# Kernel tuning notes

Measured on AMD Instinct MI355X. Metric: run time of the kernel, lower is better.

Reference implementation:

```python
import jax, jax.numpy as jnp
import numpy as np

BLOCK_SIZE = 8
SELECT_TOPK = 32
HIDDEN = 512
CHANNELS = 384
NUM_HEADS = 8
B, H, W = 8, 64, 64


def setup_inputs() -> dict:
    key = jax.random.key(0)
    ks = jax.random.split(key, 8)
    num_block_tot = (H // BLOCK_SIZE) * (W // BLOCK_SIZE)
    bs2 = BLOCK_SIZE * BLOCK_SIZE
    x = jax.random.normal(ks[0], (B, H, W, CHANNELS), dtype=jnp.float32)
    aw = jax.random.normal(ks[1], (NUM_HEADS, B, num_block_tot, bs2, bs2 + SELECT_TOPK), dtype=jnp.float32)
    attn_weights = jax.nn.softmax(aw, axis=-1)  # module expects sum(-1)==1
    weights = jax.random.uniform(ks[2], (B, num_block_tot, SELECT_TOPK), dtype=jnp.float32)
    indexes = jax.random.randint(ks[3], (B, num_block_tot, SELECT_TOPK), 0, H * W)
    in_proj_w = jax.random.normal(ks[4], (3 * HIDDEN, CHANNELS), dtype=jnp.float32) * 0.02
    in_proj_b = jax.random.normal(ks[5], (3 * HIDDEN,), dtype=jnp.float32) * 0.02
    out_proj_w = jax.random.normal(ks[6], (CHANNELS, HIDDEN), dtype=jnp.float32) * 0.02
    out_proj_b = jax.random.normal(ks[7], (CHANNELS,), dtype=jnp.float32) * 0.02
    return {"x": x, "attn_weights": attn_weights, "weights": weights,
            "in_proj_w": in_proj_w, "in_proj_b": in_proj_b,
            "out_proj_w": out_proj_w, "out_proj_b": out_proj_b,
            "indexes": indexes}


def reference(x, attn_weights, weights, in_proj_w, in_proj_b, out_proj_w, out_proj_b, indexes):
    batch, height, width, _ = x.shape
    bsz = BLOCK_SIZE
    nbh, nbw = height // bsz, width // bsz
    nbt = nbh * nbw
    num_heads = attn_weights.shape[0]
    hid = HIDDEN
    hd = hid // num_heads
    topk = SELECT_TOPK

    proj = jnp.einsum('bhwc,oc->bhwo', x, in_proj_w) + in_proj_b  # (B,H,W,3*hid)
    s, xh, y = jnp.split(proj, 3, axis=-1)
    xh = xh * jnp.tanh(s)  # Balancer/Whiten/Identity are identity in fwd

    # top-k gathered tokens: (B, nbt, topk, hid) without (B,nbt,num_tokens,hid) blowup
    x_flat = xh.reshape(batch, height * width, hid)
    sel = jax.vmap(lambda xf, ix: xf[ix])(x_flat, indexes)  # (B,nbt,topk,hid)
    sel = sel * weights[..., None]
    sel = sel.reshape(batch, nbt, topk, num_heads, hd).transpose(3, 0, 1, 2, 4)  # (nh,B,nbt,topk,hd)

    # block-local tokens: (nh, B, nbt, bsz^2, hd)
    blk = xh.reshape(batch, nbh, bsz, nbw, bsz, num_heads, hd)
    blk = blk.transpose(5, 0, 1, 3, 2, 4, 6).reshape(num_heads, batch, nbt, bsz * bsz, hd)

    kv = jnp.concatenate([blk, sel], axis=3)  # (nh,B,nbt,bsz^2+topk,hd)
    out = jnp.einsum('hbnqk,hbnkd->hbnqd', attn_weights, kv)  # (nh,B,nbt,bsz^2,hd)

    out = out.reshape(num_heads, batch, nbh, nbw, bsz, bsz, hd)
    out = out.transpose(1, 2, 4, 3, 5, 0, 6).reshape(batch, height, width, hid)
    out = out * y
    return jnp.einsum('bhwd,cd->bhwc', out, out_proj_w) + out_proj_b
```

## Files before the change

### kernel.cpp

```cpp
#include <hip/hip_runtime.h>
#include <hip/hip_bf16.h>
#include <stdint.h>

#define CH   384
#define HID  512
#define NHD  8
#define MTOT 32768

typedef __attribute__((ext_vector_type(8))) short bf16x8;
typedef __attribute__((ext_vector_type(4))) float f32x4;
typedef unsigned short u16;

__device__ __forceinline__ float bf2f(u16 v){ return __uint_as_float(((unsigned)v)<<16); }
__device__ __forceinline__ u16 f2bf(float f){
  unsigned u = __float_as_uint(f);
  return (u16)((u + 0x7fffu + ((u>>16)&1u)) >> 16);
}
__device__ __forceinline__ void gload_lds16(const void* g, void* l){
  __builtin_amdgcn_global_load_lds((const __attribute__((address_space(1))) void*)g,
                                   (__attribute__((address_space(3))) void*)l, 16, 0, 0);
}

__global__ void k_cvt(const float* __restrict__ in, u16* __restrict__ out, int n4){
  int i = blockIdx.x*blockDim.x + threadIdx.x;
  int stride = gridDim.x*blockDim.x;
  for (; i < n4; i += stride){
    float4 v = ((const float4*)in)[i];
    ushort4 o; o.x=f2bf(v.x); o.y=f2bf(v.y); o.z=f2bf(v.z); o.w=f2bf(v.w);
    ((ushort4*)out)[i] = o;
  }
}

__global__ __launch_bounds__(256)
void k_gemm1(const u16* __restrict__ xb, const u16* __restrict__ w1b,
             const float* __restrict__ b1,
             u16* __restrict__ xh, u16* __restrict__ yb)
{
  __shared__ short lds[40960];
  const int tid = threadIdx.x;
  const int w = tid >> 6, lw = tid & 63;
  const int wm = w >> 1, wn = w & 1;
  const int bid = blockIdx.x;
  const int xcd = bid & 7, ii = bid >> 3;
  const int m0 = (xcd*32 + (ii >> 3)) * 128;
  const int h0 = (ii & 7) * 64;
  const int lc = lw & 15, lk = lw >> 4;

  f32x4 acc[4][6] = {};

  const int sl = (lw & 7) ^ (lw >> 3);
  const int rsub = lw >> 3;
  const u16* gsrc[10]; int ldst[10];
  #pragma unroll
  for (int i = 0; i < 10; ++i){
    int c = w*10 + i;
    if (c < 16){
      int r = c*8 + rsub;
      gsrc[i] = xb + (size_t)(m0 + r)*CH + sl*8;
      ldst[i] = c*512;
    } else {
      int cb = c - 16;
      int rb = cb*8 + rsub;
      int hb = rb/48, rem = rb - hb*48;
      int seg = rem >> 4, iw = rem & 15;
      gsrc[i] = w1b + (size_t)(seg*HID + h0 + hb*16 + iw)*CH + sl*8;
      ldst[i] = 8192 + cb*512;
    }
  }
  auto STAGE = [&](int buf, int kt){
    #pragma unroll
    for (int i = 0; i < 10; ++i)
      gload_lds16(gsrc[i] + kt*64, &lds[ldst[i] + buf*20480]);
  };
  auto COMPUTE = [&](int buf){
    const short* pa = lds + buf*20480;
    const short* pb = lds + buf*20480 + 8192;
    #pragma unroll
    for (int ks = 0; ks < 2; ++ks){
      bf16x8 af[4], bv[6];
      #pragma unroll
      for (int mi = 0; mi < 4; ++mi){
        int row = wm*64 + mi*16 + lc;
        int s = (ks*4 + lk) ^ (lc & 7);
        af[mi] = *(const bf16x8*)&pa[row*64 + s*8];
      }
      #pragma unroll
      for (int nj = 0; nj < 6; ++nj){
        int row = wn*96 + (nj/3)*48 + (nj%3)*16 + lc;
        int s = (ks*4 + lk) ^ (lc & 7);
        bv[nj] = *(const bf16x8*)&pb[row*64 + s*8];
      }
      #pragma unroll
      for (int mi = 0; mi < 4; ++mi)
        #pragma unroll
        for (int nj = 0; nj < 6; ++nj)
          acc[mi][nj] = __builtin_amdgcn_mfma_f32_16x16x32_bf16(af[mi], bv[nj], acc[mi][nj], 0,0,0);
    }
  };

  STAGE(0, 0);
  #pragma unroll 1
  for (int kt = 0; kt < 6; ++kt){
    if (kt < 5){
      STAGE((kt+1)&1, kt+1);
      asm volatile("s_waitcnt vmcnt(10)" ::: "memory");
    } else {
      asm volatile("s_waitcnt vmcnt(0)" ::: "memory");
    }
    __builtin_amdgcn_sched_barrier(0);
    __builtin_amdgcn_s_barrier();
    COMPUTE(kt&1);
    __builtin_amdgcn_sched_barrier(0);
    __builtin_amdgcn_s_barrier();
  }

  {
    short* ep  = &lds[w*2560];
    short* ep2 = &lds[10240 + w*2560];
    const int gr = m0 + wm*64 + lw;
    const int gc = h0 + wn*32;
    float bs[2], bx[2], by[2];
    #pragma unroll
    for (int hb = 0; hb < 2; ++hb){
      int col = gc + hb*16 + lc;
      bs[hb] = b1[col]; bx[hb] = b1[512 + col]; by[hb] = b1[1024 + col];
    }
    #pragma unroll
    for (int mi = 0; mi < 4; ++mi)
      #pragma unroll
      for (int hb = 0; hb < 2; ++hb)
        #pragma unroll
        for (int j = 0; j < 4; ++j){
          float sv = acc[mi][hb*3 + 0][j] + bs[hb];
          float xv = (acc[mi][hb*3 + 1][j] + bx[hb]) * tanhf(sv);
          float yv = acc[mi][hb*3 + 2][j] + by[hb];
          int row = mi*16 + lk*4 + j;
          ep [row*40 + hb*16 + lc] = (short)f2bf(xv);
          ep2[row*40 + hb*16 + lc] = (short)f2bf(yv);
        }
    __syncthreads();
    #pragma unroll
    for (int q = 0; q < 4; ++q){
      bf16x8 v = *(const bf16x8*)&ep[lw*40 + q*8];
      *(bf16x8*)&xh[(size_t)gr*HID + gc + q*8] = v;
    }
    #pragma unroll
    for (int q = 0; q < 4; ++q){
      bf16x8 v = *(const bf16x8*)&ep2[lw*40 + q*8];
      *(bf16x8*)&yb[(size_t)gr*HID + gc + q*8] = v;
    }
  }
}

__global__ __launch_bounds__(64, 3)
void k_attn(const float* __restrict__ aw, const float* __restrict__ wts,
            const int* __restrict__ idxs,
            const u16* __restrict__ xh, const u16* __restrict__ yb,
            u16* __restrict__ zb)
{
  __shared__ short lKv[64*96];
  const int tid = threadIdx.x;
  const int bid = blockIdx.x;
  const int h = bid >> 9;
  const int b = (bid >> 6) & 7;
  const int n = bid & 63;
  const int bh = n >> 3, bw = n & 7;

  {
    const int dg = tid & 7;
    const int pr = tid >> 3;
    #pragma unroll
    for (int it = 0; it < 6; ++it){
      int pair = it*8 + pr;
      int t0 = pair*2;
      size_t r0, r1;
      if (t0 < 64){
        int pix = (bh*8 + (t0>>3))*64 + bw*8 + (t0&7);
        r0 = (size_t)b*4096 + pix;
        r1 = r0 + 1;
      } else {
        int e = (b*64+n)*32 + (t0-64);
        r0 = (size_t)b*4096 + idxs[e];
        r1 = (size_t)b*4096 + idxs[e+1];
      }
      bf16x8 v0 = *(const bf16x8*)&xh[r0*HID + h*64 + dg*8];
      bf16x8 v1 = *(const bf16x8*)&xh[r1*HID + h*64 + dg*8];
      #pragma unroll
      for (int j = 0; j < 8; ++j){
        int d = dg*8 + j;
        int elem = (d*96 + t0) ^ (dg<<3);
        unsigned pk = (unsigned)(u16)v0[j] | ((unsigned)(u16)v1[j] << 16);
        *(unsigned*)&lKv[elem] = pk;
      }
    }
  }

  float wv[8];
  {
    const float* wp = wts + (size_t)(b*64+n)*32 + (tid>>4)*8;
    float4 a = *(const float4*)wp, c = *(const float4*)(wp+4);
    wv[0]=a.x; wv[1]=a.y; wv[2]=a.z; wv[3]=a.w;
    wv[4]=c.x; wv[5]=c.y; wv[6]=c.z; wv[7]=c.w;
  }
  const float* awp = aw + (size_t)bid * (64*96);
  bf16x8 af[3][4];
  #pragma unroll
  for (int ks = 0; ks < 3; ++ks){
    #pragma unroll
    for (int mi = 0; mi < 4; ++mi){
      const float* p = awp + (size_t)(mi*16 + (tid&15))*96 + ks*32 + (tid>>4)*8;
      float4 f0 = *(const float4*)p;
      float4 f1 = *(const float4*)(p+4);
      float t[8] = {f0.x,f0.y,f0.z,f0.w,f1.x,f1.y,f1.z,f1.w};
      #pragma unroll
      for (int j = 0; j < 8; ++j){
        float v = (ks == 2) ? t[j]*wv[j] : t[j];
        af[ks][mi][j] = (short)f2bf(v);
      }
    }
  }
  __syncthreads();

  f32x4 acc[4][4] = {};
  const int lc = tid & 15, lk = tid >> 4;
  #pragma unroll
  for (int ks = 0; ks < 3; ++ks){
    bf16x8 bv[4];
    #pragma unroll
    for (int nj = 0; nj < 4; ++nj){
      int d = nj*16 + lc;
      int idx = (d*96 + ks*32 + lk*8) ^ ((d>>3)<<3);
      bv[nj] = *(const bf16x8*)&lKv[idx];
    }
    #pragma unroll
    for (int mi = 0; mi < 4; ++mi)
      #pragma unroll
      for (int nj = 0; nj < 4; ++nj)
        acc[mi][nj] = __builtin_amdgcn_mfma_f32_16x16x32_bf16(af[ks][mi], bv[nj], acc[mi][nj], 0,0,0);
  }

  #pragma unroll
  for (int mi = 0; mi < 4; ++mi){
    #pragma unroll
    for (int nj = 0; nj < 4; ++nj){
      int d = nj*16 + lc;
      size_t gcol = (size_t)h*64 + d;
      #pragma unroll
      for (int j = 0; j < 4; ++j){
        int q = mi*16 + lk*4 + j;
        int pix = (bh*8 + (q>>3))*64 + bw*8 + (q&7);
        size_t r = (size_t)b*4096 + pix;
        float yv = bf2f(yb[r*HID + gcol]);
        zb[r*HID + gcol] = f2bf(acc[mi][nj][j] * yv);
      }
    }
  }
}

__global__ __launch_bounds__(256)
void k_gemm2(const u16* __restrict__ zb, const u16* __restrict__ w2b,
             const float* __restrict__ b2, float* __restrict__ out)
{
  __shared__ short lds[32768];
  const int tid = threadIdx.x;
  const int w = tid>>6, lw = tid&63;
  const int wm = w>>1, wn = w&1;
  const int bid = blockIdx.x;
  const int xcd = bid & 7, ii = bid >> 3;
  const int m0 = (xcd*32 + ii/3) * 128;
  const int n0 = (ii%3) * 128;

  f32x4 acc[4][4] = {};

  const int sl = (lw&7) ^ (lw>>3);
  const int rsub = lw >> 3;
  const u16* gA[4]; const u16* gB[4]; int lA[4], lB[4];
  #pragma unroll
  for (int i = 0; i < 4; ++i){
    int c = i*4 + w;
    int r = c*8 + rsub;
    gA[i] = zb  + (size_t)(m0+r)*HID + sl*8;
    gB[i] = w2b + (size_t)(n0+r)*HID + sl*8;
    lA[i] = c*512; lB[i] = 8192 + c*512;
  }
  auto STAGE = [&](int buf, int kt){
    #pragma unroll
    for (int i = 0; i < 4; ++i){
      gload_lds16(gA[i] + kt*64, &lds[lA[i] + buf*16384]);
      gload_lds16(gB[i] + kt*64, &lds[lB[i] + buf*16384]);
    }
  };
  auto COMPUTE = [&](int buf){
    const short* pa = lds + buf*16384;
    const short* pb = lds + buf*16384 + 8192;
    #pragma unroll
    for (int ks=0; ks<2; ++ks){
      bf16x8 af[4], bb[4];
      #pragma unroll
      for (int mi=0; mi<4; ++mi){
        int row = wm*64 + mi*16 + (lw&15);
        int s = (ks*4 + (lw>>4)) ^ (row&7);
        af[mi] = *(const bf16x8*)&pa[row*64 + s*8];
      }
      #pragma unroll
      for (int nj=0; nj<4; ++nj){
        int row = wn*64 + nj*16 + (lw&15);
        int s = (ks*4 + (lw>>4)) ^ (row&7);
        bb[nj] = *(const bf16x8*)&pb[row*64 + s*8];
      }
      #pragma unroll
      for (int mi=0; mi<4; ++mi)
        #pragma unroll
        for (int nj=0; nj<4; ++nj)
          acc[mi][nj] = __builtin_amdgcn_mfma_f32_16x16x32_bf16(af[mi], bb[nj], acc[mi][nj], 0,0,0);
    }
  };

  STAGE(0, 0);
  #pragma unroll 1
  for (int kt = 0; kt < 8; ++kt){
    if (kt < 7){
      STAGE((kt+1)&1, kt+1);
      asm volatile("s_waitcnt vmcnt(8)" ::: "memory");
    } else {
      asm volatile("s_waitcnt vmcnt(0)" ::: "memory");
    }
    __builtin_amdgcn_sched_barrier(0);
    __builtin_amdgcn_s_barrier();
    COMPUTE(kt&1);
    __builtin_amdgcn_sched_barrier(0);
    __builtin_amdgcn_s_barrier();
  }

  const int lc = lw&15, lr4 = (lw>>4)*4;
  #pragma unroll
  for (int nj=0; nj<4; ++nj){
    int col = n0 + wn*64 + nj*16 + lc;
    float bias = b2[col];
    #pragma unroll
    for (int mi=0; mi<4; ++mi){
      #pragma unroll
      for (int j=0; j<4; ++j){
        int row = m0 + wm*64 + mi*16 + lr4 + j;
        out[(size_t)row*CH + col] = acc[mi][nj][j] + bias;
      }
    }
  }
}

extern "C" void kernel_launch(void* const* d_in, const int* in_sizes, int n_in,
                              void* d_out, int out_size, void* d_ws, size_t ws_size,
                              hipStream_t stream) {
  const float* x   = (const float*)d_in[0];
  const float* aw  = (const float*)d_in[1];
  const float* wts = (const float*)d_in[2];
  const float* w1  = (const float*)d_in[3];
  const float* b1  = (const float*)d_in[4];
  const float* w2  = (const float*)d_in[5];
  const float* b2  = (const float*)d_in[6];
  const int*   idx = (const int*)d_in[7];
  float* out = (float*)d_out;

  char* ws = (char*)d_ws;
  u16* x_bf  = (u16*)(ws);
  u16* w1_bf = (u16*)(ws + 25165824);
  u16* w2_bf = (u16*)(ws + 26345472);
  u16* xh_bf = (u16*)(ws + 26738688);
  u16* y_bf  = (u16*)(ws + 60293120);
  u16* z_bf  = (u16*)(ws + 93847552);

  k_cvt<<<2048, 256, 0, stream>>>(x,  x_bf,  MTOT*CH/4);
  k_cvt<<<576,  256, 0, stream>>>(w1, w1_bf, 3*HID*CH/4);
  k_cvt<<<192,  256, 0, stream>>>(w2, w2_bf, CH*HID/4);

  k_gemm1<<<2048, 256, 0, stream>>>(x_bf, w1_bf, b1, xh_bf, y_bf);
  k_attn<<<NHD*8*64, 64, 0, stream>>>(aw, wts, idx, xh_bf, y_bf, z_bf);
  k_gemm2<<<768, 256, 0, stream>>>(z_bf, w2_bf, b2, out);
}
```

Measured before the change: 158.5 us.

## Halve K-tile in both GEMMs to cut LDS and raise occupancy; fast tanh

Both bf16 MFMA GEMMs now stage 32-wide K tiles instead of 64-wide. This halves LDS per block, adds a new swizzle for 4 chunks per row, and doubles the number of K iterations. Launch bounds now request 4 blocks per SM so more blocks can be resident to hide memory latency. The cost is twice as many barriers per GEMM. The gemm1 epilogue also replaces tanhf with an exp plus reciprocal approximation, which may shift accuracy slightly.

After: 190.7 us. +20.3%, slower.

```diff
diff --git a/kernel.cpp b/kernel.cpp
--- a/kernel.cpp
+++ b/kernel.cpp
@@ -15,6 +15,10 @@
 __device__ __forceinline__ u16 f2bf(float f){
   unsigned u = __float_as_uint(f);
   return (u16)((u + 0x7fffu + ((u>>16)&1u)) >> 16);
+}
+__device__ __forceinline__ float fast_tanh(float s){
+  float e = __expf(2.f*s);
+  return 1.f - 2.f*__builtin_amdgcn_rcpf(e + 1.f);
 }
 __device__ __forceinline__ void gload_lds16(const void* g, void* l){
   __builtin_amdgcn_global_load_lds((const __attribute__((address_space(1))) void*)g,
@@ -31,12 +35,12 @@
   }
 }
 
-__global__ __launch_bounds__(256)
+__global__ __launch_bounds__(256, 4)
 void k_gemm1(const u16* __restrict__ xb, const u16* __restrict__ w1b,
              const float* __restrict__ b1,
              u16* __restrict__ xh, u16* __restrict__ yb)
 {
-  __shared__ short lds[40960];
+  __shared__ short lds[20480];
   const int tid = threadIdx.x;
   const int w = tid >> 6, lw = tid & 63;
   const int wm = w >> 1, wn = w & 1;
@@ -48,62 +52,58 @@
 
   f32x4 acc[4][6] = {};
 
-  const int sl = (lw & 7) ^ (lw >> 3);
-  const int rsub = lw >> 3;
-  const u16* gsrc[10]; int ldst[10];
-  #pragma unroll
-  for (int i = 0; i < 10; ++i){
-    int c = w*10 + i;
-    if (c < 16){
-      int r = c*8 + rsub;
-      gsrc[i] = xb + (size_t)(m0 + r)*CH + sl*8;
+  const int sl_g = (lw & 3) ^ ((lw >> 3) & 3);
+  const int rsub = lw >> 2;
+  const u16* gsrc[5]; int ldst[5];
+  #pragma unroll
+  for (int i = 0; i < 5; ++i){
+    int c = w*5 + i;
+    if (c < 8){
+      int r = c*16 + rsub;
+      gsrc[i] = xb + (size_t)(m0 + r)*CH + sl_g*8;
       ldst[i] = c*512;
     } else {
-      int cb = c - 16;
-      int rb = cb*8 + rsub;
+      int cb = c - 8;
+      int rb = cb*16 + rsub;
       int hb = rb/48, rem = rb - hb*48;
       int seg = rem >> 4, iw = rem & 15;
-      gsrc[i] = w1b + (size_t)(seg*HID + h0 + hb*16 + iw)*CH + sl*8;
-      ldst[i] = 8192 + cb*512;
+      gsrc[i] = w1b + (size_t)(seg*HID + h0 + hb*16 + iw)*CH + sl_g*8;
+      ldst[i] = 4096 + cb*512;
     }
   }
   auto STAGE = [&](int buf, int kt){
     #pragma unroll
-    for (int i = 0; i < 10; ++i)
-      gload_lds16(gsrc[i] + kt*64, &lds[ldst[i] + buf*20480]);
+    for (int i = 0; i < 5; ++i)
+      gload_lds16(gsrc[i] + kt*32, &lds[ldst[i] + buf*10240]);
   };
+  const int skey = (lc >> 1) & 3;
   auto COMPUTE = [&](int buf){
-    const short* pa = lds + buf*20480;
-    const short* pb = lds + buf*20480 + 8192;
-    #pragma unroll
-    for (int ks = 0; ks < 2; ++ks){
-      bf16x8 af[4], bv[6];
-      #pragma unroll
-      for (int mi = 0; mi < 4; ++mi){
-        int row = wm*64 + mi*16 + lc;
-        int s = (ks*4 + lk) ^ (lc & 7);
-        af[mi] = *(const bf16x8*)&pa[row*64 + s*8];
-      }
-      #pragma unroll
-      for (int nj = 0; nj < 6; ++nj){
-        int row = wn*96 + (nj/3)*48 + (nj%3)*16 + lc;
-        int s = (ks*4 + lk) ^ (lc & 7);
-        bv[nj] = *(const bf16x8*)&pb[row*64 + s*8];
-      }
-      #pragma unroll
-      for (int mi = 0; mi < 4; ++mi)
-        #pragma unroll
-        for (int nj = 0; nj < 6; ++nj)
-          acc[mi][nj] = __builtin_amdgcn_mfma_f32_16x16x32_bf16(af[mi], bv[nj], acc[mi][nj], 0,0,0);
-    }
+    const short* pa = lds + buf*10240;
+    const short* pb = lds + buf*10240 + 4096;
+    bf16x8 af[4], bv[6];
+    #pragma unroll
+    for (int mi = 0; mi < 4; ++mi){
+      int row = wm*64 + mi*16 + lc;
+      af[mi] = *(const bf16x8*)&pa[row*32 + (lk ^ skey)*8];
+    }
+    #pragma unroll
+    for (int nj = 0; nj < 6; ++nj){
+      int row = wn*96 + (nj/3)*48 + (nj%3)*16 + lc;
+      bv[nj] = *(const bf16x8*)&pb[row*32 + (lk ^ skey)*8];
+    }
+    #pragma unroll
+    for (int mi = 0; mi < 4; ++mi)
+      #pragma unroll
+      for (int nj = 0; nj < 6; ++nj)
+        acc[mi][nj] = __builtin_amdgcn_mfma_f32_16x16x32_bf16(af[mi], bv[nj], acc[mi][nj], 0,0,0);
   };
 
   STAGE(0, 0);
   #pragma unroll 1
-  for (int kt = 0; kt < 6; ++kt){
-    if (kt < 5){
+  for (int kt = 0; kt < 12; ++kt){
+    if (kt < 11){
       STAGE((kt+1)&1, kt+1);
-      asm volatile("s_waitcnt vmcnt(10)" ::: "memory");
+      asm volatile("s_waitcnt vmcnt(5)" ::: "memory");
     } else {
       asm volatile("s_waitcnt vmcnt(0)" ::: "memory");
     }
@@ -132,7 +132,7 @@
         #pragma unroll
         for (int j = 0; j < 4; ++j){
           float sv = acc[mi][hb*3 + 0][j] + bs[hb];
-          float xv = (acc[mi][hb*3 + 1][j] + bx[hb]) * tanhf(sv);
+          float xv = (acc[mi][hb*3 + 1][j] + bx[hb]) * fast_tanh(sv);
           float yv = acc[mi][hb*3 + 2][j] + by[hb];
           int row = mi*16 + lk*4 + j;
           ep [row*40 + hb*16 + lc] = (short)f2bf(xv);
@@ -257,11 +257,11 @@
   }
 }
 
-__global__ __launch_bounds__(256)
+__global__ __launch_bounds__(256, 4)
 void k_gemm2(const u16* __restrict__ zb, const u16* __restrict__ w2b,
              const float* __restrict__ b2, float* __restrict__ out)
 {
-  __shared__ short lds[32768];
+  __shared__ short lds[16384];
   const int tid = threadIdx.x;
   const int w = tid>>6, lw = tid&63;
   const int wm = w>>1, wn = w&1;
@@ -269,59 +269,60 @@
   const int xcd = bid & 7, ii = bid >> 3;
   const int m0 = (xcd*32 + ii/3) * 128;
   const int n0 = (ii%3) * 128;
+  const int lc = lw & 15, lk = lw >> 4;
 
   f32x4 acc[4][4] = {};
 
-  const int sl = (lw&7) ^ (lw>>3);
-  const int rsub = lw >> 3;
-  const u16* gA[4]; const u16* gB[4]; int lA[4], lB[4];
+  const int sl_g = (lw & 3) ^ ((lw >> 3) & 3);
+  const int rsub = lw >> 2;
+  const u16* gsrc[4]; int ldst[4];
   #pragma unroll
   for (int i = 0; i < 4; ++i){
-    int c = i*4 + w;
-    int r = c*8 + rsub;
-    gA[i] = zb  + (size_t)(m0+r)*HID + sl*8;
-    gB[i] = w2b + (size_t)(n0+r)*HID + sl*8;
-    lA[i] = c*512; lB[i] = 8192 + c*512;
+    int c = w*4 + i;
+    if (c < 8){
+      int r = c*16 + rsub;
+      gsrc[i] = zb + (size_t)(m0+r)*HID + sl_g*8;
+      ldst[i] = c*512;
+    } else {
+      int cb = c - 8;
+      int r = cb*16 + rsub;
+      gsrc[i] = w2b + (size_t)(n0+r)*HID + sl_g*8;
+      ldst[i] = 4096 + cb*512;
+    }
   }
   auto STAGE = [&](int buf, int kt){
     #pragma unroll
-    for (int i = 0; i < 4; ++i){
-      gload_lds16(gA[i] + kt*64, &lds[lA[i] + buf*16384]);
-      gload_lds16(gB[i] + kt*64, &lds[lB[i] + buf*16384]);
-    }
+    for (int i = 0; i < 4; ++i)
+      gload_lds16(gsrc[i] + kt*32, &lds[ldst[i] + buf*8192]);
   };
+  const int skey = (lc >> 1) & 3;
   auto COMPUTE = [&](int buf){
-    const short* pa = lds + buf*16384;
-    const short* pb = lds + buf*16384 + 8192;
-    #pragma unroll
-    for (int ks=0; ks<2; ++ks){
-      bf16x8 af[4], bb[4];
-      #pragma unroll
-      for (int mi=0; mi<4; ++mi){
-        int row = wm*64 + mi*16 + (lw&15);
-        int s = (ks*4 + (lw>>4)) ^ (row&7);
-        af[mi] = *(const bf16x8*)&pa[row*64 + s*8];
-      }
-      #pragma unroll
-      for (int nj=0; nj<4; ++nj){
-        int row = wn*64 + nj*16 + (lw&15);
-        int s = (ks*4 + (lw>>4)) ^ (row&7);
-        bb[nj] = *(const bf16x8*)&pb[row*64 + s*8];
-      }
-      #pragma unroll
-      for (int mi=0; mi<4; ++mi)
-        #pragma unroll
-        for (int nj=0; nj<4; ++nj)
-          acc[mi][nj] = __builtin_amdgcn_mfma_f32_16x16x32_bf16(af[mi], bb[nj], acc[mi][nj], 0,0,0);
-    }
+    const short* pa = lds + buf*8192;
+    const short* pb = lds + buf*8192 + 4096;
+    bf16x8 af[4], bb[4];
+    #pragma unroll
+    for (int mi=0; mi<4; ++mi){
+      int row = wm*64 + mi*16 + lc;
+      af[mi] = *(const bf16x8*)&pa[row*32 + (lk ^ skey)*8];
+    }
+    #pragma unroll
+    for (int nj=0; nj<4; ++nj){
+      int row = wn*64 + nj*16 + lc;
+      bb[nj] = *(const bf16x8*)&pb[row*32 + (lk ^ skey)*8];
+    }
+    #pragma unroll
+    for (int mi=0; mi<4; ++mi)
+      #pragma unroll
+      for (int nj=0; nj<4; ++nj)
+        acc[mi][nj] = __builtin_amdgcn_mfma_f32_16x16x32_bf16(af[mi], bb[nj], acc[mi][nj], 0,0,0);
   };
 
   STAGE(0, 0);
   #pragma unroll 1
-  for (int kt = 0; kt < 8; ++kt){
-    if (kt < 7){
+  for (int kt = 0; kt < 16; ++kt){
+    if (kt < 15){
       STAGE((kt+1)&1, kt+1);
-      asm volatile("s_waitcnt vmcnt(8)" ::: "memory");
+      asm volatile("s_waitcnt vmcnt(4)" ::: "memory");
     } else {
       asm volatile("s_waitcnt vmcnt(0)" ::: "memory");
     }
@@ -332,7 +333,7 @@
     __builtin_amdgcn_s_barrier();
   }
 
-  const int lc = lw&15, lr4 = (lw>>4)*4;
+  const int lr4 = lk*4;
   #pragma unroll
   for (int nj=0; nj<4; ++nj){
     int col = n0 + wn*64 + nj*16 + lc;
```
